# Kernel optimization log

Hardware: AMD Instinct MI355X
Metric: run time of the kernel (lower is better)

Reference implementation:

```python
import jax, jax.numpy as jnp
import numpy as np
from jax import lax

WIRES = 4
EPS = 1e-5


def _conv2d(x, w, b):
    # x: [B,C,H,W], w: [O,I,3,3], SAME padding, stride 1
    y = lax.conv_general_dilated(x, w, (1, 1), 'SAME',
                                 dimension_numbers=('NCHW', 'OIHW', 'NCHW'))
    return y + b[None, :, None, None]


def _maxpool2(x):
    return lax.reduce_window(x, -jnp.inf, lax.max, (1, 1, 2, 2), (1, 1, 2, 2), 'VALID')


def _cnot_perm(c, t, n=WIRES):
    # wire 0 = most significant bit; CNOT is a self-inverse basis permutation
    idx = np.arange(2 ** n)
    cbit = (idx >> (n - 1 - c)) & 1
    flipped = idx ^ (1 << (n - 1 - t))
    return np.where(cbit == 1, flipped, idx)


_CNOT_PERMS = [_cnot_perm(c, c + 1) for c in range(WIRES - 1)]
_Z_SIGNS = np.stack([1.0 - 2.0 * ((np.arange(2 ** WIRES) >> (WIRES - 1 - i)) & 1)
                     for i in range(WIRES)], axis=1).astype(np.float32)  # [16, 4]


def _quantum_circuit(q_params, feats):
    # Batched state-vector sim of: RY(feats[i]) wire i; RX(params[i]) wire i;
    # CNOT chain; <Z_i>.  feats: [B,4], q_params: [4]
    hf = 0.5 * feats
    hp = 0.5 * q_params
    cy, sy = jnp.cos(hf), jnp.sin(hf)            # [B,4]
    cx, sx = jnp.cos(hp), jnp.sin(hp)            # [4]
    # per-wire state after RX @ RY |0>: amplitudes of |0>, |1>
    a0 = (cx * cy - 1j * sx * sy).astype(jnp.complex64)  # [B,4]
    a1 = (cx * sy - 1j * sx * cy).astype(jnp.complex64)  # [B,4]
    single = jnp.stack([a0, a1], axis=-1)        # [B,4,2]
    # product state -> full 16-dim state via successive outer products
    psi = single[:, 0]                           # [B,2]
    for i in range(1, WIRES):
        psi = (psi[:, :, None] * single[:, i][:, None, :]).reshape(psi.shape[0], -1)
    # CNOT chain = fixed basis permutations
    for perm in _CNOT_PERMS:
        psi = psi[:, perm]                       # [B,16]
    probs = psi.real ** 2 + psi.imag ** 2        # [B,16]
    return probs @ jnp.asarray(_Z_SIGNS)         # [B,4]


def setup_inputs() -> dict:
    key = jax.random.key(0)
    ks = jax.random.split(key, 8)
    B, C, H, W = 512, 1, 128, 128
    return {
        'x': jax.random.normal(ks[0], (B, C, H, W), jnp.float32),
        'conv1_w': jax.random.normal(ks[1], (8, C, 3, 3), jnp.float32) * 0.1,
        'conv1_b': jnp.zeros((8,), jnp.float32),
        'conv2_w': jax.random.normal(ks[2], (16, 8, 3, 3), jnp.float32) * 0.1,
        'conv2_b': jnp.zeros((16,), jnp.float32),
        'q_params': jax.random.normal(ks[3], (WIRES,), jnp.float32),
        'bn_gamma': jnp.ones((4,), jnp.float32),
        'bn_beta': jnp.zeros((4,), jnp.float32),
        'head_w': jax.random.normal(ks[4], (4, WIRES), jnp.float32) * 0.5,
        'head_b': jnp.zeros((4,), jnp.float32),
    }


def reference(x, conv1_w, conv1_b, conv2_w, conv2_b, q_params,
              bn_gamma, bn_beta, head_w, head_b):
    h = jax.nn.relu(_conv2d(x, conv1_w, conv1_b))
    h = _maxpool2(h)
    h = jax.nn.relu(_conv2d(h, conv2_w, conv2_b))
    h = _maxpool2(h)
    feats = h.mean(axis=(2, 3))                  # AdaptiveAvgPool2d(1) -> [B,16]
    q_out = _quantum_circuit(q_params, feats[:, :WIRES])  # [B,4]
    # BatchNorm1d (training mode, biased variance)
    mu = q_out.mean(axis=0)
    var = q_out.var(axis=0)
    normed = bn_gamma * (q_out - mu) / jnp.sqrt(var + EPS) + bn_beta
    return normed @ head_w.T + head_b
```

## Files before the change

### kernel.cpp

```cpp
#include <hip/hip_runtime.h>

#define EPS 1e-5f

typedef float f2 __attribute__((ext_vector_type(2)));
typedef float f4 __attribute__((ext_vector_type(4)));

__device__ __forceinline__ float uload(const float* __restrict__ p) {
  return __int_as_float(__builtin_amdgcn_readfirstlane(__float_as_int(*p)));
}

__device__ __forceinline__ f2 fma2(f2 a, f2 b, f2 c) {
  return __builtin_elementwise_fma(a, b, c);
}
__device__ __forceinline__ f2 splat2(float s) { f2 r; r.x = s; r.y = s; return r; }

__global__ __launch_bounds__(256, 4) void k12_fused(
    const float* __restrict__ x, const float* __restrict__ w1,
    const float* __restrict__ b1, const float* __restrict__ w2,
    const float* __restrict__ b2, float* __restrict__ partials) {
  __shared__ float p1[8][18][66];
  __shared__ float w1t[80];
  __shared__ float w2t[292];
  __shared__ float wred[4][4];

  const int q   = blockIdx.x & 3;
  const int b   = blockIdx.x >> 2;
  const int tid = threadIdx.x;
  const float* xb = x + (size_t)b * (128 * 128);

  if (tid < 72) {
    int oc = tid / 9, k = tid % 9;
    w1t[k * 8 + oc] = w1[tid];
  } else if (tid < 80) {
    w1t[tid] = b1[tid - 72];
  }
  {
    int t = tid;
    {
      int oc = t / 72, rem = t % 72, ic = rem / 9, k = rem % 9;
      w2t[(ic * 9 + k) * 4 + oc] = w2[t];
    }
    t = tid + 256;
    if (t < 288) {
      int oc = t / 72, rem = t % 72, ic = rem / 9, k = rem % 9;
      w2t[(ic * 9 + k) * 4 + oc] = w2[t];
    }
  }
  if (tid >= 80 && tid < 84) w2t[288 + tid - 80] = b2[tid - 80];
  if (tid >= 96 && tid < 240) {
    int t = tid - 96;
    int ic = t / 18, r = t % 18;
    p1[ic][r][0]  = 0.f;
    p1[ic][r][65] = 0.f;
  }
  __syncthreads();

#pragma unroll 1
  for (int pos = tid; pos < 576; pos += 256) {
    const int gl = pos >> 5, i = pos & 31;
    const int G  = 16 * q - 1 + gl;
    const bool vG = ((unsigned)G) < 64u;
    const int xr0 = 2 * G - 1;
    float xin[4][6];
#pragma unroll
    for (int r = 0; r < 4; ++r) {
      const int row  = xr0 + r;
      const bool rok = vG && ((unsigned)row < 128u);
      const int rowc = min(max(row, 0), 127);
      const float* rp = xb + rowc * 128;
      const float le = rp[(i == 0) ? 0 : (4 * i - 1)];
      const f4 mid   = *(const f4*)(rp + 4 * i);
      const float ri = rp[(i == 31) ? 127 : (4 * i + 4)];
      xin[r][0] = (rok && i != 0)  ? le    : 0.f;
      xin[r][1] = rok              ? mid.x : 0.f;
      xin[r][2] = rok              ? mid.y : 0.f;
      xin[r][3] = rok              ? mid.z : 0.f;
      xin[r][4] = rok              ? mid.w : 0.f;
      xin[r][5] = (rok && i != 31) ? ri    : 0.f;
    }
#pragma unroll 1
    for (int g = 0; g < 2; ++g) {
      f2 wpx[9][2], bias1[2];
#pragma unroll
      for (int k = 0; k < 9; ++k) {
        wpx[k][0] = *(const f2*)&w1t[k * 8 + 4 * g];
        wpx[k][1] = *(const f2*)&w1t[k * 8 + 4 * g + 2];
      }
      bias1[0] = *(const f2*)&w1t[72 + 4 * g];
      bias1[1] = *(const f2*)&w1t[72 + 4 * g + 2];
#pragma unroll
      for (int p = 0; p < 2; ++p)
#pragma unroll
        for (int h = 0; h < 2; ++h) {
          f2 best = splat2(0.f);
#pragma unroll
          for (int dy = 0; dy < 2; ++dy)
#pragma unroll
            for (int dx = 0; dx < 2; ++dx) {
              f2 a = bias1[p];
#pragma unroll
              for (int ky = 0; ky < 3; ++ky)
#pragma unroll
                for (int kx = 0; kx < 3; ++kx)
                  a = fma2(wpx[ky * 3 + kx][p],
                           splat2(xin[dy + ky][2 * h + dx + kx]), a);
              best.x = fmaxf(best.x, a.x);
              best.y = fmaxf(best.y, a.y);
            }
          const int oc0 = 4 * g + 2 * p;
          p1[oc0][gl][2 * i + 1 + h]     = vG ? best.x : 0.f;
          p1[oc0 + 1][gl][2 * i + 1 + h] = vG ? best.y : 0.f;
        }
    }
  }
  __syncthreads();

  const int px2  = tid & 31;
  const int py2l = tid >> 5;

  f2 acc[2][2][2];
#pragma unroll
  for (int p = 0; p < 2; ++p) {
    const f2 bias = *(const f2*)&w2t[288 + 2 * p];
    acc[p][0][0] = bias; acc[p][0][1] = bias;
    acc[p][1][0] = bias; acc[p][1][1] = bias;
  }

#pragma unroll 1
  for (int ic = 0; ic < 8; ++ic) {
    float xin[4][4];
#pragma unroll
    for (int r = 0; r < 4; ++r) {
      const f2* rp = (const f2*)&p1[ic][2 * py2l + r][2 * px2];
      f2 v0 = rp[0], v1 = rp[1];
      xin[r][0] = v0.x; xin[r][1] = v0.y; xin[r][2] = v1.x; xin[r][3] = v1.y;
    }
#pragma unroll
    for (int ky = 0; ky < 3; ++ky)
#pragma unroll
      for (int kx = 0; kx < 3; ++kx) {
        const int k = ky * 3 + kx;
        const f2 w0  = *(const f2*)&w2t[(ic * 9 + k) * 4];
        const f2 w1p = *(const f2*)&w2t[(ic * 9 + k) * 4 + 2];
#pragma unroll
        for (int dy = 0; dy < 2; ++dy)
#pragma unroll
          for (int dx = 0; dx < 2; ++dx) {
            const f2 xs = splat2(xin[dy + ky][dx + kx]);
            acc[0][dy][dx] = fma2(w0, xs, acc[0][dy][dx]);
            acc[1][dy][dx] = fma2(w1p, xs, acc[1][dy][dx]);
          }
      }
  }

  const int lane = tid & 63, w = tid >> 6;
#pragma unroll
  for (int p = 0; p < 2; ++p) {
    f2 m01;
    m01.x = fmaxf(fmaxf(fmaxf(acc[p][0][0].x, acc[p][0][1].x),
                        fmaxf(acc[p][1][0].x, acc[p][1][1].x)), 0.f);
    m01.y = fmaxf(fmaxf(fmaxf(acc[p][0][0].y, acc[p][0][1].y),
                        fmaxf(acc[p][1][0].y, acc[p][1][1].y)), 0.f);
#pragma unroll
    for (int off = 32; off > 0; off >>= 1) {
      m01.x += __shfl_down(m01.x, off);
      m01.y += __shfl_down(m01.y, off);
    }
    if (lane == 0) { wred[w][2 * p] = m01.x; wred[w][2 * p + 1] = m01.y; }
  }
  __syncthreads();
  if (tid < 4) {
    float s = wred[0][tid] + wred[1][tid] + wred[2][tid] + wred[3][tid];
    partials[((size_t)b * 4 + q) * 4 + tid] = s;
  }
}

__global__ __launch_bounds__(512) void k3_tail(
    const float* __restrict__ partials, const float* __restrict__ qp,
    const float* __restrict__ gamma, const float* __restrict__ beta,
    const float* __restrict__ hw, const float* __restrict__ hb,
    float* __restrict__ out) {
  __shared__ float wsum[8][8];
  __shared__ float stats[8];
  const int tid = threadIdx.x;

  const f4* pp = (const f4*)(partials + tid * 16);
  f4 s0 = pp[0], s1 = pp[1], s2 = pp[2], s3 = pp[3];
  float f[4];
  f[0] = (s0.x + s1.x + s2.x + s3.x) * (1.f / 1024.f);
  f[1] = (s0.y + s1.y + s2.y + s3.y) * (1.f / 1024.f);
  f[2] = (s0.z + s1.z + s2.z + s3.z) * (1.f / 1024.f);
  f[3] = (s0.w + s1.w + s2.w + s3.w) * (1.f / 1024.f);

  float a0r[4], a0i[4], a1r[4], a1i[4];
#pragma unroll
  for (int i = 0; i < 4; ++i) {
    float cy, sy, cx, sx;
    __sincosf(0.5f * f[i], &sy, &cy);
    __sincosf(0.5f * uload(qp + i), &sx, &cx);
    a0r[i] = cx * cy; a0i[i] = -sx * sy;
    a1r[i] = cx * sy; a1i[i] = -sx * cy;
  }

  float pr[16], pi[16];
#pragma unroll
  for (int j = 0; j < 16; ++j) {
    float rr = 1.f, ii = 0.f;
#pragma unroll
    for (int w = 0; w < 4; ++w) {
      int bit = (j >> (3 - w)) & 1;
      float ar = bit ? a1r[w] : a0r[w];
      float ai = bit ? a1i[w] : a0i[w];
      float t = rr * ar - ii * ai;
      ii = rr * ai + ii * ar;
      rr = t;
    }
    pr[j] = rr; pi[j] = ii;
  }

  constexpr int comp[16] = {0, 1, 3, 2, 6, 7, 5, 4, 12, 13, 15, 14, 10, 11, 9, 8};
  float qv[4] = {0.f, 0.f, 0.f, 0.f};
#pragma unroll
  for (int j = 0; j < 16; ++j) {
    int s = comp[j];
    float p = pr[s] * pr[s] + pi[s] * pi[s];
#pragma unroll
    for (int i = 0; i < 4; ++i)
      qv[i] += ((j >> (3 - i)) & 1) ? -p : p;
  }

  float v[8];
#pragma unroll
  for (int i = 0; i < 4; ++i) { v[i] = qv[i]; v[4 + i] = qv[i] * qv[i]; }
#pragma unroll
  for (int k = 0; k < 8; ++k)
#pragma unroll
    for (int off = 32; off > 0; off >>= 1) v[k] += __shfl_down(v[k], off);
  const int lane = tid & 63, w = tid >> 6;
  if (lane == 0) {
#pragma unroll
    for (int k = 0; k < 8; ++k) wsum[w][k] = v[k];
  }
  __syncthreads();
  if (tid < 8) {
    float s = 0.f;
#pragma unroll
    for (int ww = 0; ww < 8; ++ww) s += wsum[ww][tid];
    stats[tid] = s * (1.f / 512.f);
  }
  __syncthreads();

  float nm[4];
#pragma unroll
  for (int i = 0; i < 4; ++i) {
    float mu  = stats[i];
    float var = stats[4 + i] - mu * mu;
    nm[i] = uload(gamma + i) * (qv[i] - mu) * rsqrtf(var + EPS) + uload(beta + i);
  }
#pragma unroll
  for (int k = 0; k < 4; ++k) {
    float o = uload(hb + k);
#pragma unroll
    for (int i = 0; i < 4; ++i) o = fmaf(nm[i], uload(hw + k * 4 + i), o);
    out[tid * 4 + k] = o;
  }
}

extern "C" void kernel_launch(void* const* d_in, const int* in_sizes, int n_in,
                              void* d_out, int out_size, void* d_ws, size_t ws_size,
                              hipStream_t stream) {
  const float* x  = (const float*)d_in[0];
  const float* w1 = (const float*)d_in[1];
  const float* b1 = (const float*)d_in[2];
  const float* w2 = (const float*)d_in[3];
  const float* b2 = (const float*)d_in[4];
  const float* qp = (const float*)d_in[5];
  const float* gm = (const float*)d_in[6];
  const float* bt = (const float*)d_in[7];
  const float* hw = (const float*)d_in[8];
  const float* hb = (const float*)d_in[9];
  float* out = (float*)d_out;

  float* partials = (float*)d_ws;

  k12_fused<<<512 * 4, 256, 0, stream>>>(x, w1, b1, w2, b2, partials);
  k3_tail<<<1, 512, 0, stream>>>(partials, qp, gm, bt, hw, hb, out);
}
```

Before: 121.0 us.

## Fuse tail kernel into conv kernel via last-block atomic counter

Removes the separate single-block tail kernel launch and folds the quantum-circuit, batchnorm and head computation into the main conv kernel. Blocks increment a global counter and the last block to finish (detected via atomicAdd with threadfences) runs the tail with 256 threads, each processing two batch rows. This avoids one kernel launch and its gap, at the cost of an extra memset launch for the counter, extra shared memory and registers in the main kernel, and a serialized tail executed by one block.

```diff
diff --git a/kernel.cpp b/kernel.cpp
--- a/kernel.cpp
+++ b/kernel.cpp
@@ -17,11 +17,18 @@
 __global__ __launch_bounds__(256, 4) void k12_fused(
     const float* __restrict__ x, const float* __restrict__ w1,
     const float* __restrict__ b1, const float* __restrict__ w2,
-    const float* __restrict__ b2, float* __restrict__ partials) {
+    const float* __restrict__ b2, float* __restrict__ partials,
+    unsigned int* __restrict__ counter, const float* __restrict__ qp,
+    const float* __restrict__ gamma, const float* __restrict__ beta,
+    const float* __restrict__ hw, const float* __restrict__ hb,
+    float* __restrict__ out) {
   __shared__ float p1[8][18][66];
   __shared__ float w1t[80];
   __shared__ float w2t[292];
   __shared__ float wred[4][4];
+  __shared__ float tsum[4][8];
+  __shared__ float tstats[8];
+  __shared__ bool  is_last;
 
   const int q   = blockIdx.x & 3;
   const int b   = blockIdx.x >> 2;
@@ -173,96 +180,109 @@
     float s = wred[0][tid] + wred[1][tid] + wred[2][tid] + wred[3][tid];
     partials[((size_t)b * 4 + q) * 4 + tid] = s;
   }
-}
-
-__global__ __launch_bounds__(512) void k3_tail(
-    const float* __restrict__ partials, const float* __restrict__ qp,
-    const float* __restrict__ gamma, const float* __restrict__ beta,
-    const float* __restrict__ hw, const float* __restrict__ hb,
-    float* __restrict__ out) {
-  __shared__ float wsum[8][8];
-  __shared__ float stats[8];
-  const int tid = threadIdx.x;
-
-  const f4* pp = (const f4*)(partials + tid * 16);
-  f4 s0 = pp[0], s1 = pp[1], s2 = pp[2], s3 = pp[3];
-  float f[4];
-  f[0] = (s0.x + s1.x + s2.x + s3.x) * (1.f / 1024.f);
-  f[1] = (s0.y + s1.y + s2.y + s3.y) * (1.f / 1024.f);
-  f[2] = (s0.z + s1.z + s2.z + s3.z) * (1.f / 1024.f);
-  f[3] = (s0.w + s1.w + s2.w + s3.w) * (1.f / 1024.f);
-
-  float a0r[4], a0i[4], a1r[4], a1i[4];
-#pragma unroll
-  for (int i = 0; i < 4; ++i) {
-    float cy, sy, cx, sx;
-    __sincosf(0.5f * f[i], &sy, &cy);
-    __sincosf(0.5f * uload(qp + i), &sx, &cx);
-    a0r[i] = cx * cy; a0i[i] = -sx * sy;
-    a1r[i] = cx * sy; a1i[i] = -sx * cy;
-  }
-
-  float pr[16], pi[16];
-#pragma unroll
-  for (int j = 0; j < 16; ++j) {
-    float rr = 1.f, ii = 0.f;
-#pragma unroll
-    for (int w = 0; w < 4; ++w) {
-      int bit = (j >> (3 - w)) & 1;
-      float ar = bit ? a1r[w] : a0r[w];
-      float ai = bit ? a1i[w] : a0i[w];
-      float t = rr * ar - ii * ai;
-      ii = rr * ai + ii * ar;
-      rr = t;
-    }
-    pr[j] = rr; pi[j] = ii;
-  }
-
-  constexpr int comp[16] = {0, 1, 3, 2, 6, 7, 5, 4, 12, 13, 15, 14, 10, 11, 9, 8};
-  float qv[4] = {0.f, 0.f, 0.f, 0.f};
-#pragma unroll
-  for (int j = 0; j < 16; ++j) {
-    int s = comp[j];
-    float p = pr[s] * pr[s] + pi[s] * pi[s];
-#pragma unroll
-    for (int i = 0; i < 4; ++i)
-      qv[i] += ((j >> (3 - i)) & 1) ? -p : p;
-  }
-
+
+  if (tid == 0) {
+    __threadfence();
+    unsigned int prev = atomicAdd(counter, 1u);
+    is_last = (prev == 2047u);
+  }
+  __syncthreads();
+  if (!is_last) return;
+  __threadfence();
+
+  float qv2[2][4];
   float v[8];
 #pragma unroll
-  for (int i = 0; i < 4; ++i) { v[i] = qv[i]; v[4 + i] = qv[i] * qv[i]; }
+  for (int k = 0; k < 8; ++k) v[k] = 0.f;
+
+#pragma unroll 1
+  for (int half = 0; half < 2; ++half) {
+    const int bt = tid + half * 256;
+    const f4* pp = (const f4*)(partials + bt * 16);
+    f4 s0 = pp[0], s1 = pp[1], s2 = pp[2], s3 = pp[3];
+    float f[4];
+    f[0] = (s0.x + s1.x + s2.x + s3.x) * (1.f / 1024.f);
+    f[1] = (s0.y + s1.y + s2.y + s3.y) * (1.f / 1024.f);
+    f[2] = (s0.z + s1.z + s2.z + s3.z) * (1.f / 1024.f);
+    f[3] = (s0.w + s1.w + s2.w + s3.w) * (1.f / 1024.f);
+
+    float a0r[4], a0i[4], a1r[4], a1i[4];
+#pragma unroll
+    for (int i = 0; i < 4; ++i) {
+      float cy, sy, cx, sx;
+      __sincosf(0.5f * f[i], &sy, &cy);
+      __sincosf(0.5f * uload(qp + i), &sx, &cx);
+      a0r[i] = cx * cy; a0i[i] = -sx * sy;
+      a1r[i] = cx * sy; a1i[i] = -sx * cy;
+    }
+
+    float pr[16], pi[16];
+#pragma unroll
+    for (int j = 0; j < 16; ++j) {
+      float rr = 1.f, ii = 0.f;
+#pragma unroll
+      for (int wi = 0; wi < 4; ++wi) {
+        int bit = (j >> (3 - wi)) & 1;
+        float ar = bit ? a1r[wi] : a0r[wi];
+        float ai = bit ? a1i[wi] : a0i[wi];
+        float t = rr * ar - ii * ai;
+        ii = rr * ai + ii * ar;
+        rr = t;
+      }
+      pr[j] = rr; pi[j] = ii;
+    }
+
+    constexpr int comp[16] = {0, 1, 3, 2, 6, 7, 5, 4, 12, 13, 15, 14, 10, 11, 9, 8};
+#pragma unroll
+    for (int i = 0; i < 4; ++i) qv2[half][i] = 0.f;
+#pragma unroll
+    for (int j = 0; j < 16; ++j) {
+      int s = comp[j];
+      float p = pr[s] * pr[s] + pi[s] * pi[s];
+#pragma unroll
+      for (int i = 0; i < 4; ++i)
+        qv2[half][i] += ((j >> (3 - i)) & 1) ? -p : p;
+    }
+#pragma unroll
+    for (int i = 0; i < 4; ++i) {
+      v[i]     += qv2[half][i];
+      v[4 + i] += qv2[half][i] * qv2[half][i];
+    }
+  }
+
 #pragma unroll
   for (int k = 0; k < 8; ++k)
 #pragma unroll
     for (int off = 32; off > 0; off >>= 1) v[k] += __shfl_down(v[k], off);
-  const int lane = tid & 63, w = tid >> 6;
   if (lane == 0) {
 #pragma unroll
-    for (int k = 0; k < 8; ++k) wsum[w][k] = v[k];
+    for (int k = 0; k < 8; ++k) tsum[w][k] = v[k];
   }
   __syncthreads();
   if (tid < 8) {
-    float s = 0.f;
-#pragma unroll
-    for (int ww = 0; ww < 8; ++ww) s += wsum[ww][tid];
-    stats[tid] = s * (1.f / 512.f);
-  }
-  __syncthreads();
-
-  float nm[4];
-#pragma unroll
-  for (int i = 0; i < 4; ++i) {
-    float mu  = stats[i];
-    float var = stats[4 + i] - mu * mu;
-    nm[i] = uload(gamma + i) * (qv[i] - mu) * rsqrtf(var + EPS) + uload(beta + i);
-  }
-#pragma unroll
-  for (int k = 0; k < 4; ++k) {
-    float o = uload(hb + k);
-#pragma unroll
-    for (int i = 0; i < 4; ++i) o = fmaf(nm[i], uload(hw + k * 4 + i), o);
-    out[tid * 4 + k] = o;
+    float s = tsum[0][tid] + tsum[1][tid] + tsum[2][tid] + tsum[3][tid];
+    tstats[tid] = s * (1.f / 512.f);
+  }
+  __syncthreads();
+
+#pragma unroll 1
+  for (int half = 0; half < 2; ++half) {
+    const int bt = tid + half * 256;
+    float nm[4];
+#pragma unroll
+    for (int i = 0; i < 4; ++i) {
+      float mu  = tstats[i];
+      float var = tstats[4 + i] - mu * mu;
+      nm[i] = uload(gamma + i) * (qv2[half][i] - mu) * rsqrtf(var + EPS) +
+              uload(beta + i);
+    }
+#pragma unroll
+    for (int k = 0; k < 4; ++k) {
+      float o = uload(hb + k);
+#pragma unroll
+      for (int i = 0; i < 4; ++i) o = fmaf(nm[i], uload(hw + k * 4 + i), o);
+      out[bt * 4 + k] = o;
+    }
   }
 }
 
@@ -282,7 +302,9 @@
   float* out = (float*)d_out;
 
   float* partials = (float*)d_ws;
-
-  k12_fused<<<512 * 4, 256, 0, stream>>>(x, w1, b1, w2, b2, partials);
-  k3_tail<<<1, 512, 0, stream>>>(partials, qp, gm, bt, hw, hb, out);
+  unsigned int* counter = (unsigned int*)((char*)d_ws + (32 << 10));
+
+  hipMemsetAsync(counter, 0, sizeof(unsigned int), stream);
+  k12_fused<<<512 * 4, 256, 0, stream>>>(x, w1, b1, w2, b2, partials, counter,
+                                         qp, gm, bt, hw, hb, out);
 }
```

Measured after the change: 149.2 us. 23.2% more time.
